# Kernel tuning notes

Measured on AMD Instinct MI355X. Metric: run time of the kernel, lower is better.

The kernel has to match this reference:

```python
import jax, jax.numpy as jnp
import numpy as np

B, S, D, H, F = 4, 1024, 512, 8, 2048
EPS = 1e-6


def _layernorm(x, g, b):
    m = jnp.mean(x, axis=-1, keepdims=True)
    v = jnp.mean(jnp.square(x - m), axis=-1, keepdims=True)
    return (x - m) * jax.lax.rsqrt(v + EPS) * g + b


def setup_inputs() -> dict:
    key = jax.random.key(0)
    ks = jax.random.split(key, 16)
    sd = 0.02
    return {
        "input_tensor": jax.random.normal(ks[0], (B, S, D), jnp.float32),
        # per-head QKV projections: each head maps D -> D (full depth, as in source)
        "Wq": jax.random.normal(ks[1], (H, D, D), jnp.float32) * sd,
        "bq": jnp.zeros((H, D), jnp.float32),
        "Wk": jax.random.normal(ks[2], (H, D, D), jnp.float32) * sd,
        "bk": jnp.zeros((H, D), jnp.float32),
        "Wv": jax.random.normal(ks[3], (H, D, D), jnp.float32) * sd,
        "bv": jnp.zeros((H, D), jnp.float32),
        # output projection after concat of H full-depth heads: (H*D) -> D
        "Wo": jax.random.normal(ks[4], (H * D, D), jnp.float32) * sd,
        "bo": jnp.zeros((D,), jnp.float32),
        "g1": jnp.ones((D,), jnp.float32),
        "beta1": jnp.zeros((D,), jnp.float32),
        "W1": jax.random.normal(ks[5], (D, F), jnp.float32) * sd,
        "b1": jnp.zeros((F,), jnp.float32),
        "W2": jax.random.normal(ks[6], (F, D), jnp.float32) * sd,
        "b2": jnp.zeros((D,), jnp.float32),
        "g2": jnp.ones((D,), jnp.float32),
        "beta2": jnp.zeros((D,), jnp.float32),
    }


def reference(input_tensor, Wq, bq, Wk, bk, Wv, bv, Wo, bo,
              g1, beta1, W1, b1, W2, b2, g2, beta2):
    x = input_tensor
    # batched per-head projections: [B,S,D] x [H,D,E] -> [B,H,S,E]
    q = jnp.einsum("bsd,hde->bhse", x, Wq) + bq[None, :, None, :]
    k = jnp.einsum("bsd,hde->bhse", x, Wk) + bk[None, :, None, :]
    v = jnp.einsum("bsd,hde->bhse", x, Wv) + bv[None, :, None, :]
    scale = 1.0 / jnp.sqrt(jnp.asarray(D, x.dtype))
    scores = jnp.einsum("bhse,bhte->bhst", q, k) * scale  # [B,H,S,S]
    attn = jax.nn.softmax(scores, axis=-1)
    heads = jnp.einsum("bhst,bhte->bhse", attn, v)  # [B,H,S,E]
    # concat heads on last axis: [B,S,H*D]
    concat = jnp.transpose(heads, (0, 2, 1, 3)).reshape(B, S, H * D)
    mha = concat @ Wo + bo  # [B,S,D]
    # dropout is identity at inference
    y = _layernorm(x + mha, g1, beta1)
    ff = jax.nn.relu(y @ W1 + b1) @ W2 + b2
    return _layernorm(y + ff, g2, beta2)
```

## Files before the change

kernel.cpp:

```cpp
#include <hip/hip_runtime.h>
#include <hip/hip_bf16.h>

typedef unsigned short u16;
typedef unsigned int u32;
typedef __attribute__((ext_vector_type(4))) float f32x4;
typedef __attribute__((ext_vector_type(8))) __bf16 bf16x8;

#define DEV __device__ __forceinline__

DEV u16 f2bf(float f) {
  union { float f; unsigned u; } c; c.f = f;
  unsigned r = (c.u + 0x7fffu + ((c.u >> 16) & 1u)) >> 16;
  return (u16)r;
}

DEV float bf2f(u16 u) {
  union { u32 u; float f; } c; c.u = (u32)u << 16;
  return c.f;
}

DEV void gld_lds16(const void* g, void* l) {
  __builtin_amdgcn_global_load_lds(
      (__attribute__((address_space(1))) void*)g,
      (__attribute__((address_space(3))) void*)l, 16, 0, 0);
}

DEV f32x4 mfma_bf16(bf16x8 a, bf16x8 b, f32x4 c) {
  return __builtin_amdgcn_mfma_f32_16x16x32_bf16(a, b, c, 0, 0, 0);
}

DEV void bar_vm0() { asm volatile("s_waitcnt vmcnt(0) lgkmcnt(0)\n\ts_barrier" ::: "memory"); }
DEV void wait_lg0() { asm volatile("s_waitcnt lgkmcnt(0)" ::: "memory"); }

DEV u32 cvt_pk_bf16(float lo, float hi) {
  u32 d;
  asm("v_cvt_pk_bf16_f32 %0, %1, %2" : "=v"(d) : "v"(lo), "v"(hi));
  return d;
}

__global__ __launch_bounds__(256) void prep_kernel(const float* __restrict__ x,
                                                   const float* __restrict__ Wq,
                                                   const float* __restrict__ Wk,
                                                   const float* __restrict__ Wv,
                                                   const float* __restrict__ Wo,
                                                   const float* __restrict__ W1,
                                                   const float* __restrict__ W2,
                                                   u16* __restrict__ xb, u16* __restrict__ wqC,
                                                   u16* __restrict__ wkC, u16* __restrict__ wvC,
                                                   u16* __restrict__ woT, u16* __restrict__ w1T,
                                                   u16* __restrict__ w2T) {
  int b = blockIdx.x;
  int tid = threadIdx.x;
  if (b < 8192) {
    const float* in;
    u16* out;
    int i;
    if (b < 2048) { in = x; out = xb; i = b * 256 + tid; }
    else {
      int idx = b - 2048;
      int job = idx >> 11;
      in = job == 0 ? Wq : (job == 1 ? Wk : Wv);
      out = job == 0 ? wqC : (job == 1 ? wkC : wvC);
      i = (idx & 2047) * 256 + tid;
    }
    float4 v = ((const float4*)in)[i];
    ushort4 o;
    o.x = f2bf(v.x); o.y = f2bf(v.y); o.z = f2bf(v.z); o.w = f2bf(v.w);
    ((ushort4*)out)[i] = o;
    return;
  }
  int idx = b - 8192;
  const float* in;
  u16* out;
  int R, C, bx, by;
  if (idx < 2048) { in = Wo; out = woT; R = 4096; C = 512; by = idx >> 4; bx = idx & 15; }
  else if (idx < 3072) { int rr = idx - 2048; in = W1; out = w1T; R = 512; C = 2048; by = rr >> 6; bx = rr & 63; }
  else { int rr = idx - 3072; in = W2; out = w2T; R = 2048; C = 512; by = rr >> 4; bx = rr & 15; }
  __shared__ float t[32][33];
  int c0 = bx * 32, r0 = by * 32;
  int tx = tid & 31, ty = tid >> 5;
#pragma unroll
  for (int i = 0; i < 4; ++i) {
    int rr2 = ty + i * 8;
    t[rr2][tx] = in[(size_t)(r0 + rr2) * C + c0 + tx];
  }
  __syncthreads();
#pragma unroll
  for (int i = 0; i < 4; ++i) {
    int cc = ty + i * 8;
    out[(size_t)(c0 + cc) * R + r0 + tx] = f2bf(t[tx][cc]);
  }
}

__global__ __launch_bounds__(256) void biasp_kernel(const float* __restrict__ Wo,
                                                    const float* __restrict__ bv,
                                                    float* __restrict__ biasP) {
  int b = blockIdx.x;
  int h = b >> 2, ec = b & 3;
  int t = threadIdx.x;
  int tl = t & 127, half = t >> 7;
  int e = ec * 128 + tl;
  float acc = 0.f;
  for (int i = 0; i < 256; ++i) {
    int e2 = half * 256 + i;
    acc += Wo[(size_t)(h * 512 + e2) * 512 + e] * bv[h * 512 + e2];
  }
  __shared__ float sh[2][128];
  sh[half][tl] = acc;
  __syncthreads();
  if (half == 0) biasP[h * 512 + e] = sh[0][tl] + sh[1][tl];
}

template <int AMODE>
__global__ __launch_bounds__(256) void gemm_bat(const u16* __restrict__ A,
                                                const u16* __restrict__ B,
                                                u16* __restrict__ out) {
  constexpr int BK = 64, BM = 128, BN = 128;
  __shared__ u16 As[2][BM * BK];
  __shared__ u16 Bs[2][BN * BK];
  const int tid = threadIdx.x;
  const int wave = tid >> 6, lane = tid & 63;
  const int r = lane & 15, g = lane >> 4;
  const int row0 = blockIdx.y * BM, col0 = blockIdx.x * BN;
  const int head = row0 >> 9;
  const int wr = (wave >> 1) * 64, wc = (wave & 1) * 64;

  auto stage = [&](int kt, int p) {
#pragma unroll
    for (int i = 0; i < 4; ++i) {
      int bi = i * 256 + wave * 64;
      int c = bi + lane;
      int row = c >> 3, ch = (c & 7) ^ (row & 7);
      size_t aoff;
      if constexpr (AMODE == 0)
        aoff = (size_t)(row0 + row) * 512 + kt + ch * 8;
      else
        aoff = (size_t)((row0 + row) & 511) * 4096 + head * 512 + kt + ch * 8;
      gld_lds16(A + aoff, &As[p][(size_t)bi * 8]);
    }
#pragma unroll
    for (int i = 0; i < 4; ++i) {
      int bi = i * 256 + wave * 64;
      int c = bi + lane;
      int row = c >> 3, ch = (c & 7) ^ (row & 7);
      gld_lds16(B + (size_t)(head * 512 + col0 + row) * 512 + kt + ch * 8,
                &Bs[p][(size_t)bi * 8]);
    }
  };

  f32x4 acc[4][4] = {};
  stage(0, 0);
  for (int t = 0; t < 8; ++t) {
    const int p = t & 1;
    bar_vm0();
    if (t < 7) stage((t + 1) * BK, p ^ 1);
    __builtin_amdgcn_s_setprio(1);
#pragma unroll
    for (int kk = 0; kk < 2; ++kk) {
      bf16x8 af[4], bfv[4];
#pragma unroll
      for (int m = 0; m < 4; ++m)
        af[m] = *(const bf16x8*)(&As[p][(wr + m * 16 + r) * BK + (((kk * 4 + g) ^ (r & 7))) * 8]);
#pragma unroll
      for (int n = 0; n < 4; ++n)
        bfv[n] = *(const bf16x8*)(&Bs[p][(wc + n * 16 + r) * BK + (((kk * 4 + g) ^ (r & 7))) * 8]);
#pragma unroll
      for (int m = 0; m < 4; ++m)
#pragma unroll
        for (int n = 0; n < 4; ++n)
          acc[m][n] = mfma_bf16(af[m], bfv[n], acc[m][n]);
    }
    __builtin_amdgcn_s_setprio(0);
  }
#pragma unroll
  for (int m = 0; m < 4; ++m)
#pragma unroll
    for (int n = 0; n < 4; ++n)
#pragma unroll
      for (int j = 0; j < 4; ++j)
        out[(size_t)(row0 + wr + m * 16 + g * 4 + j) * 512 + col0 + wc + n * 16 + r] =
            f2bf(acc[m][n][j]);
}

template <int NT, int BM, int BN, int WM, int WN, int MODE, int SPLITK>
__global__ __launch_bounds__(NT) void gemm_tn(const u16* __restrict__ A,
                                              const u16* __restrict__ B, int N, int K,
                                              void* __restrict__ out0, void* __restrict__ out1,
                                              const float* __restrict__ bias0,
                                              const float* __restrict__ bias1) {
  constexpr int BK = 64;
  constexpr int MF = WM / 16, NF = WN / 16;
  constexpr int WC = BN / WN;
  constexpr int AI = (BM * BK / 8) / NT;
  constexpr int BI = (BN * BK / 8) / NT;
  __shared__ u16 As[2][BM * BK];
  __shared__ u16 Bs[2][BN * BK];
  const int tid = threadIdx.x;
  const int wave = tid >> 6, lane = tid & 63;
  const int r = lane & 15, g = lane >> 4;
  const int row0 = blockIdx.y * BM, col0 = blockIdx.x * BN;
  const int wr = (wave / WC) * WM, wc = (wave % WC) * WN;
  const int KS = K * SPLITK;
  const int kb0 = blockIdx.z * K;

  auto stage = [&](int kt, int p) {
#pragma unroll
    for (int i = 0; i < AI; ++i) {
      int bi = i * NT + wave * 64;
      int c = bi + lane;
      int row = c >> 3, ch = (c & 7) ^ (row & 7);
      gld_lds16(A + (size_t)(row0 + row) * KS + kb0 + kt + ch * 8, &As[p][(size_t)bi * 8]);
    }
#pragma unroll
    for (int i = 0; i < BI; ++i) {
      int bi = i * NT + wave * 64;
      int c = bi + lane;
      int row = c >> 3, ch = (c & 7) ^ (row & 7);
      gld_lds16(B + (size_t)(col0 + row) * KS + kb0 + kt + ch * 8, &Bs[p][(size_t)bi * 8]);
    }
  };

  f32x4 acc[MF][NF] = {};
  const int nt = K / BK;

  stage(0, 0);
  for (int t = 0; t < nt; ++t) {
    const int p = t & 1;
    bar_vm0();
    if (t + 1 < nt) stage((t + 1) * BK, p ^ 1);
    __builtin_amdgcn_s_setprio(1);
#pragma unroll
    for (int kk = 0; kk < 2; ++kk) {
      bf16x8 af[MF], bfv[NF];
#pragma unroll
      for (int m = 0; m < MF; ++m)
        af[m] = *(const bf16x8*)(&As[p][(wr + m * 16 + r) * BK + (((kk * 4 + g) ^ (r & 7))) * 8]);
#pragma unroll
      for (int n = 0; n < NF; ++n)
        bfv[n] = *(const bf16x8*)(&Bs[p][(wc + n * 16 + r) * BK + (((kk * 4 + g) ^ (r & 7))) * 8]);
#pragma unroll
      for (int m = 0; m < MF; ++m)
#pragma unroll
        for (int n = 0; n < NF; ++n)
          acc[m][n] = mfma_bf16(af[m], bfv[n], acc[m][n]);
    }
    __builtin_amdgcn_s_setprio(0);
  }

  const size_t moff = (size_t)blockIdx.z * gridDim.y * BM * N;
#pragma unroll
  for (int m = 0; m < MF; ++m) {
#pragma unroll
    for (int n = 0; n < NF; ++n) {
      int gcol = col0 + wc + n * 16 + r;
#pragma unroll
      for (int j = 0; j < 4; ++j) {
        int grow = row0 + wr + m * 16 + g * 4 + j;
        float val = acc[m][n][j];
        if constexpr (MODE == 0) {
          int he = gcol;
          val += bias0[he];
          int bb = grow >> 10, s = grow & 1023;
          size_t off = (((size_t)(bb * 8 + (he >> 9)) * 1024 + s) * 512) + (he & 511);
          ((u16*)out0)[off] = f2bf(val);
        } else if constexpr (MODE == 1) {
          val += bias0[grow];
          int bb = gcol >> 10, s = gcol & 1023;
          size_t off = (((size_t)bb * 8 + (grow >> 9)) * 512 + (grow & 511)) * 1024 + s;
          ((u16*)out0)[off] = f2bf(val);
        } else if constexpr (MODE == 2) {
          if (SPLITK == 1 || blockIdx.z == 0) val += bias0[gcol];
          ((float*)out0)[moff + (size_t)grow * N + gcol] = val;
        } else {
          float v2 = fmaxf(val + bias0[gcol], 0.0f);
          ((u16*)out0)[(size_t)grow * N + gcol] = f2bf(v2);
        }
      }
    }
  }
  (void)out1; (void)bias1;
}

__global__ __launch_bounds__(512, 2) void flash_kernel(const u16* __restrict__ qg,
                                                       const u16* __restrict__ kg,
                                                       const u16* __restrict__ vtg,
                                                       u16* __restrict__ concat) {
  constexpr float SCALE = 0.04419417382415922f;
  __shared__ u16 Ks[2][32 * 512];
  __shared__ u16 Vs[2][32 * 512];
  __shared__ u32 PsU[8][256];

  const int tid = threadIdx.x;
  const int wave = tid >> 6, lane = tid & 63;
  const int r = lane & 15, g = lane >> 4;
  const int bx = blockIdx.x;
  const int xcd = bx & 7, slot = bx >> 3;
  const int bh = xcd * 4 + (slot >> 3);
  const int qt = slot & 7;
  const int bb = bh >> 3, hh = bh & 7;
  const size_t hbase = (size_t)bh * 1024 * 512;
  const u16* qp = qg + hbase;
  const u16* kp = kg + (size_t)bb * 1024 * 512;
  const u16* vp = vtg + hbase;
  const int q0 = qt * 128;

  bf16x8 q[16];
#pragma unroll
  for (int kk = 0; kk < 16; ++kk)
    q[kk] = *(const bf16x8*)(qp + (size_t)(q0 + wave * 16 + r) * 512 + kk * 32 + g * 8);

  const int krow8 = lane >> 3, kch = (lane & 7) ^ (lane >> 3);
  const int vrow4 = lane >> 2, vch = (lane & 3) ^ ((lane >> 3) & 3);
  auto stageKV = [&](int t, int p) {
    int kv = t * 32;
#pragma unroll
    for (int j = 0; j < 4; ++j) {
      int id = wave * 4 + j;
      gld_lds16(kp + (size_t)(kv + j * 8 + krow8) * 512 + wave * 64 + kch * 8,
                &Ks[p][id * 512]);
    }
#pragma unroll
    for (int j = 0; j < 4; ++j) {
      int n = wave * 4 + j;
      gld_lds16(vp + (size_t)(n * 16 + vrow4) * 1024 + kv + vch * 8, &Vs[p][n * 512]);
    }
  };

  f32x4 o[32] = {};
  float mrun = -1e30f, lrun = 0.f;

  stageKV(0, 0);

  const int krh = (r >> 3) * 512;
  const int ke0 = (r & 7) * 64 + ((g ^ (r & 7)) * 8);
  const int ke1 = (r & 7) * 64 + (((4 + g) ^ (r & 7)) * 8);
  const int voff = (r * 4 + (g ^ ((r >> 1) & 3))) * 8;

  for (int t = 0; t < 32; ++t) {
    const int p = t & 1;
    bar_vm0();
    if (t < 31) stageKV(t + 1, p ^ 1);

    __builtin_amdgcn_s_setprio(1);
    f32x4 a0 = {}, a1 = {}, b0 = {}, b1 = {};
#pragma unroll
    for (int kc = 0; kc < 8; ++kc) {
      const u16* kb = &Ks[p][kc * 2048 + krh];
      bf16x8 kf00 = *(const bf16x8*)(kb + ke0);
      bf16x8 kf01 = *(const bf16x8*)(kb + 1024 + ke0);
      bf16x8 kf10 = *(const bf16x8*)(kb + ke1);
      bf16x8 kf11 = *(const bf16x8*)(kb + 1024 + ke1);
      a0 = mfma_bf16(kf00, q[2 * kc], a0);
      b0 = mfma_bf16(kf01, q[2 * kc], b0);
      a1 = mfma_bf16(kf10, q[2 * kc + 1], a1);
      b1 = mfma_bf16(kf11, q[2 * kc + 1], b1);
    }
    __builtin_amdgcn_s_setprio(0);
    f32x4 s0 = a0 + a1;
    f32x4 s1 = b0 + b1;

    float m8 = -1e30f;
#pragma unroll
    for (int j = 0; j < 4; ++j) {
      s0[j] *= SCALE;
      s1[j] *= SCALE;
      m8 = fmaxf(m8, fmaxf(s0[j], s1[j]));
    }
    m8 = fmaxf(m8, __shfl_xor(m8, 16));
    m8 = fmaxf(m8, __shfl_xor(m8, 32));
    if (__any(m8 - mrun > 6.0f)) {
      float mn = fmaxf(mrun, m8);
      float rs = __expf(mrun - mn);
      mrun = mn;
      lrun *= rs;
#pragma unroll
      for (int j = 0; j < 4; ++j) {
        float rsj = __shfl(rs, (lane & 48) | (g * 4 + j));
#pragma unroll
        for (int n = 0; n < 32; ++n) o[n][j] *= rsj;
      }
    }
    f32x4 p0, p1;
    float ls = 0.f;
#pragma unroll
    for (int j = 0; j < 4; ++j) {
      p0[j] = __expf(s0[j] - mrun);
      p1[j] = __expf(s1[j] - mrun);
      ls += p0[j] + p1[j];
    }
    ls += __shfl_xor(ls, 16);
    ls += __shfl_xor(ls, 32);
    lrun += ls;

    {
      u32* pw = &PsU[wave][0];
      int base = r * 4 + (g & 1) * 2 + (g >> 1) * 64;
      pw[base + 0] = cvt_pk_bf16(p0[0], p0[1]);
      pw[base + 1] = cvt_pk_bf16(p0[2], p0[3]);
      pw[base + 128 + 0] = cvt_pk_bf16(p1[0], p1[1]);
      pw[base + 128 + 1] = cvt_pk_bf16(p1[2], p1[3]);
    }
    wait_lg0();

    bf16x8 pa = *(const bf16x8*)&PsU[wave][lane * 4];
    __builtin_amdgcn_s_setprio(1);
#pragma unroll
    for (int n = 0; n < 32; ++n) {
      bf16x8 bv = *(const bf16x8*)&Vs[p][n * 512 + voff];
      o[n] = mfma_bf16(pa, bv, o[n]);
    }
    __builtin_amdgcn_s_setprio(0);
  }

  float invl = 1.0f / lrun;
#pragma unroll
  for (int j = 0; j < 4; ++j) {
    float inv = __shfl(invl, (lane & 48) | (g * 4 + j));
    int srow = q0 + wave * 16 + g * 4 + j;
    size_t rowoff = ((size_t)bb * 1024 + srow) * 4096;
#pragma unroll
    for (int n = 0; n < 32; ++n) {
      int ocol = hh * 512 + n * 16 + r;
      concat[rowoff + ocol] = f2bf(o[n][j] * inv);
    }
  }
}

__global__ __launch_bounds__(128) void add_ln_kernel(const float* __restrict__ xin,
                                                     const u16* __restrict__ cc8,
                                                     const float* __restrict__ addin,
                                                     const float* __restrict__ addin2,
                                                     const float* __restrict__ bias,
                                                     const float* __restrict__ gamma,
                                                     const float* __restrict__ beta,
                                                     float* __restrict__ yout,
                                                     u16* __restrict__ ybout) {
  int row = blockIdx.x;
  int t = threadIdx.x;
  float4 xv = ((const float4*)(xin + (size_t)row * 512))[t];
  float v0 = xv.x, v1 = xv.y, v2 = xv.z, v3 = xv.w;
  if (cc8) {
    const u16* cr = cc8 + (size_t)row * 4096 + t * 4;
#pragma unroll
    for (int h = 0; h < 8; ++h) {
      ushort4 u = *(const ushort4*)(cr + h * 512);
      v0 += bf2f(u.x); v1 += bf2f(u.y); v2 += bf2f(u.z); v3 += bf2f(u.w);
    }
  }
  if (addin) {
    float4 av = ((const float4*)(addin + (size_t)row * 512))[t];
    v0 += av.x; v1 += av.y; v2 += av.z; v3 += av.w;
  }
  if (addin2) {
    float4 bv2 = ((const float4*)(addin2 + (size_t)row * 512))[t];
    v0 += bv2.x; v1 += bv2.y; v2 += bv2.z; v3 += bv2.w;
  }
  if (bias) {
    float4 b4 = ((const float4*)bias)[t];
    v0 += b4.x; v1 += b4.y; v2 += b4.z; v3 += b4.w;
  }
  float s1 = v0 + v1 + v2 + v3;
  float s2 = v0 * v0 + v1 * v1 + v2 * v2 + v3 * v3;
#pragma unroll
  for (int d = 1; d < 64; d <<= 1) {
    s1 += __shfl_xor(s1, d);
    s2 += __shfl_xor(s2, d);
  }
  __shared__ float sh[4];
  int wv = t >> 6;
  if ((t & 63) == 0) { sh[wv * 2] = s1; sh[wv * 2 + 1] = s2; }
  __syncthreads();
  s1 = sh[0] + sh[2];
  s2 = sh[1] + sh[3];
  float mean = s1 * (1.0f / 512.0f);
  float var = s2 * (1.0f / 512.0f) - mean * mean;
  float rstd = rsqrtf(var + 1e-6f);
  float4 gv = ((const float4*)gamma)[t];
  float4 bv = ((const float4*)beta)[t];
  float o0 = (v0 - mean) * rstd * gv.x + bv.x;
  float o1 = (v1 - mean) * rstd * gv.y + bv.y;
  float o2 = (v2 - mean) * rstd * gv.z + bv.z;
  float o3 = (v3 - mean) * rstd * gv.w + bv.w;
  float4 ov; ov.x = o0; ov.y = o1; ov.z = o2; ov.w = o3;
  ((float4*)(yout + (size_t)row * 512))[t] = ov;
  if (ybout) {
    ushort4 ub;
    ub.x = f2bf(o0); ub.y = f2bf(o1); ub.z = f2bf(o2); ub.w = f2bf(o3);
    ((ushort4*)(ybout + (size_t)row * 512))[t] = ub;
  }
}

extern "C" void kernel_launch(void* const* d_in, const int* in_sizes, int n_in, void* d_out,
                              int out_size, void* d_ws, size_t ws_size, hipStream_t stream) {
  (void)in_sizes; (void)n_in; (void)out_size; (void)ws_size;
  const float* x   = (const float*)d_in[0];
  const float* Wq  = (const float*)d_in[1];
  const float* bq  = (const float*)d_in[2];
  const float* Wk  = (const float*)d_in[3];
  const float* bk  = (const float*)d_in[4];
  const float* Wv  = (const float*)d_in[5];
  const float* bv  = (const float*)d_in[6];
  const float* Wo  = (const float*)d_in[7];
  const float* bo  = (const float*)d_in[8];
  const float* g1  = (const float*)d_in[9];
  const float* be1 = (const float*)d_in[10];
  const float* W1  = (const float*)d_in[11];
  const float* b1  = (const float*)d_in[12];
  const float* W2  = (const float*)d_in[13];
  const float* b2  = (const float*)d_in[14];
  const float* g2  = (const float*)d_in[15];
  const float* be2 = (const float*)d_in[16];
  (void)bk;

  char* ws = (char*)d_ws;
  const size_t MB = 1024 * 1024;
  u16*   xb    = (u16*)(ws + 0);
  u16*   wqC   = (u16*)(ws + 4 * MB);
  u16*   wkC   = (u16*)(ws + 8 * MB);
  u16*   wvC   = (u16*)(ws + 12 * MB);
  u16*   woT   = (u16*)(ws + 16 * MB);
  u16*   w1T   = (u16*)(ws + 20 * MB);
  u16*   w2T   = (u16*)(ws + 22 * MB);
  float* biasP = (float*)(ws + 24 * MB);
  u16*   mhT   = (u16*)(ws + 26 * MB);
  u16*   nhT   = (u16*)(ws + 30 * MB);
  u16*   qb    = (u16*)(ws + 34 * MB);
  u16*   vTb   = (u16*)(ws + 66 * MB);
  u16*   cc    = (u16*)(ws + 98 * MB);
  float* y     = (float*)(ws + 4 * MB);
  u16*   yb    = (u16*)(ws + 26 * MB);
  u16*   ff1   = (u16*)(ws + 34 * MB);
  float* ff2a  = (float*)(ws + 50 * MB);
  float* ff2b  = (float*)(ws + 58 * MB);

  prep_kernel<<<12288, 256, 0, stream>>>(x, Wq, Wk, Wv, Wo, W1, W2, xb, wqC, wkC, wvC,
                                         woT, w1T, w2T);
  biasp_kernel<<<32, 256, 0, stream>>>(Wo, bv, biasP);
  gemm_bat<0><<<dim3(4, 32), 256, 0, stream>>>(wkC, wqC, mhT);
  gemm_bat<1><<<dim3(4, 32), 256, 0, stream>>>(woT, wvC, nhT);
  gemm_tn<512, 256, 256, 128, 64, 0, 1><<<dim3(16, 16), 512, 0, stream>>>(xb, mhT, 4096, 512, qb, nullptr, bq, nullptr);
  gemm_tn<512, 256, 256, 128, 64, 1, 1><<<dim3(16, 16), 512, 0, stream>>>(nhT, xb, 4096, 512, vTb, nullptr, biasP, nullptr);
  flash_kernel<<<256, 512, 0, stream>>>(qb, xb, vTb, cc);
  add_ln_kernel<<<4096, 128, 0, stream>>>(x, cc, nullptr, nullptr, bo, g1, be1, y, yb);
  gemm_tn<256, 128, 128, 64, 64, 3, 1><<<dim3(16, 32), 256, 0, stream>>>(yb, w1T, 2048, 512, ff1, nullptr, b1, nullptr);
  gemm_tn<256, 64, 128, 32, 64, 2, 2><<<dim3(4, 64, 2), 256, 0, stream>>>(ff1, w2T, 512, 1024, ff2a, nullptr, b2, nullptr);
  add_ln_kernel<<<4096, 128, 0, stream>>>(y, nullptr, ff2a, ff2b, nullptr, g2, be2, (float*)d_out, nullptr);
}
```

Measured before the change: 247.1 us.

## Use FP8 for V and softmax probabilities in flash attention PV matmul

The V projection GEMM now writes its transposed output as FP8 bytes instead of bf16. The flash kernel stages V into a half-size LDS buffer with a new swizzle, packs the probabilities P to FP8, and uses the 16x16x32 fp8 MFMA for the P·V product. This halves V traffic and LDS footprint and uses the faster fp8 matrix path. The cost is precision: FP8 probabilities and V values may raise the error against the fp32 reference.

```diff
diff --git a/kernel.cpp b/kernel.cpp
--- a/kernel.cpp
+++ b/kernel.cpp
@@ -2,7 +2,9 @@
 #include <hip/hip_bf16.h>
 
 typedef unsigned short u16;
+typedef unsigned char u8;
 typedef unsigned int u32;
+typedef long long i64;
 typedef __attribute__((ext_vector_type(4))) float f32x4;
 typedef __attribute__((ext_vector_type(8))) __bf16 bf16x8;
 
@@ -32,10 +34,15 @@
 DEV void bar_vm0() { asm volatile("s_waitcnt vmcnt(0) lgkmcnt(0)\n\ts_barrier" ::: "memory"); }
 DEV void wait_lg0() { asm volatile("s_waitcnt lgkmcnt(0)" ::: "memory"); }
 
-DEV u32 cvt_pk_bf16(float lo, float hi) {
-  u32 d;
-  asm("v_cvt_pk_bf16_f32 %0, %1, %2" : "=v"(d) : "v"(lo), "v"(hi));
-  return d;
+DEV u32 pack_fp8x4(float a, float b, float c, float d) {
+  u32 t = __builtin_amdgcn_cvt_pk_fp8_f32(a, b, 0, false);
+  t = __builtin_amdgcn_cvt_pk_fp8_f32(c, d, t, true);
+  return t;
+}
+
+DEV u8 f2fp8(float v) {
+  u32 t = __builtin_amdgcn_cvt_pk_fp8_f32(v, v, 0, false);
+  return (u8)(t & 0xff);
 }
 
 __global__ __launch_bounds__(256) void prep_kernel(const float* __restrict__ x,
@@ -185,9 +192,8 @@
 template <int NT, int BM, int BN, int WM, int WN, int MODE, int SPLITK>
 __global__ __launch_bounds__(NT) void gemm_tn(const u16* __restrict__ A,
                                               const u16* __restrict__ B, int N, int K,
-                                              void* __restrict__ out0, void* __restrict__ out1,
-                                              const float* __restrict__ bias0,
-                                              const float* __restrict__ bias1) {
+                                              void* __restrict__ out0,
+                                              const float* __restrict__ bias0) {
   constexpr int BK = 64;
   constexpr int MF = WM / 16, NF = WN / 16;
   constexpr int WC = BN / WN;
@@ -267,7 +273,7 @@
           val += bias0[grow];
           int bb = gcol >> 10, s = gcol & 1023;
           size_t off = (((size_t)bb * 8 + (grow >> 9)) * 512 + (grow & 511)) * 1024 + s;
-          ((u16*)out0)[off] = f2bf(val);
+          ((u8*)out0)[off] = f2fp8(val);
         } else if constexpr (MODE == 2) {
           if (SPLITK == 1 || blockIdx.z == 0) val += bias0[gcol];
           ((float*)out0)[moff + (size_t)grow * N + gcol] = val;
@@ -278,17 +284,16 @@
       }
     }
   }
-  (void)out1; (void)bias1;
 }
 
 __global__ __launch_bounds__(512, 2) void flash_kernel(const u16* __restrict__ qg,
                                                        const u16* __restrict__ kg,
-                                                       const u16* __restrict__ vtg,
+                                                       const u8* __restrict__ vtg,
                                                        u16* __restrict__ concat) {
   constexpr float SCALE = 0.04419417382415922f;
   __shared__ u16 Ks[2][32 * 512];
-  __shared__ u16 Vs[2][32 * 512];
-  __shared__ u32 PsU[8][256];
+  __shared__ __align__(16) u8 VsB[2][16 * 1024];
+  __shared__ __align__(16) u32 PsP[8][128];
 
   const int tid = threadIdx.x;
   const int wave = tid >> 6, lane = tid & 63;
@@ -301,7 +306,7 @@
   const size_t hbase = (size_t)bh * 1024 * 512;
   const u16* qp = qg + hbase;
   const u16* kp = kg + (size_t)bb * 1024 * 512;
-  const u16* vp = vtg + hbase;
+  const u8* vp = vtg + (size_t)bh * 512 * 1024;
   const int q0 = qt * 128;
 
   bf16x8 q[16];
@@ -310,7 +315,9 @@
     q[kk] = *(const bf16x8*)(qp + (size_t)(q0 + wave * 16 + r) * 512 + kk * 32 + g * 8);
 
   const int krow8 = lane >> 3, kch = (lane & 7) ^ (lane >> 3);
-  const int vrow4 = lane >> 2, vch = (lane & 3) ^ ((lane >> 3) & 3);
+  const int vrow_s = lane >> 1;
+  const int vsw_s = (vrow_s & 2) ^ ((vrow_s >> 2) & 2);
+  const int vhalf = lane & 1;
   auto stageKV = [&](int t, int p) {
     int kv = t * 32;
 #pragma unroll
@@ -320,9 +327,10 @@
                 &Ks[p][id * 512]);
     }
 #pragma unroll
-    for (int j = 0; j < 4; ++j) {
-      int n = wave * 4 + j;
-      gld_lds16(vp + (size_t)(n * 16 + vrow4) * 1024 + kv + vch * 8, &Vs[p][n * 512]);
+    for (int jj = 0; jj < 2; ++jj) {
+      int nv = wave * 2 + jj;
+      gld_lds16(vp + (size_t)(nv * 32 + vrow_s) * 1024 + kv + (((vhalf * 2) ^ vsw_s) * 8),
+                &VsB[p][nv * 1024]);
     }
   };
 
@@ -334,7 +342,9 @@
   const int krh = (r >> 3) * 512;
   const int ke0 = (r & 7) * 64 + ((g ^ (r & 7)) * 8);
   const int ke1 = (r & 7) * 64 + (((4 + g) ^ (r & 7)) * 8);
-  const int voff = (r * 4 + (g ^ ((r >> 1) & 3))) * 8;
+  const int vsw = (r & 2) ^ ((r >> 2) & 2);
+  const int vo8 = ((g ^ vsw) << 3);
+  const int psw = r & 6;
 
   for (int t = 0; t < 32; ++t) {
     const int p = t & 1;
@@ -393,21 +403,21 @@
     lrun += ls;
 
     {
-      u32* pw = &PsU[wave][0];
-      int base = r * 4 + (g & 1) * 2 + (g >> 1) * 64;
-      pw[base + 0] = cvt_pk_bf16(p0[0], p0[1]);
-      pw[base + 1] = cvt_pk_bf16(p0[2], p0[3]);
-      pw[base + 128 + 0] = cvt_pk_bf16(p1[0], p1[1]);
-      pw[base + 128 + 1] = cvt_pk_bf16(p1[2], p1[3]);
+      u32* pw = PsP[wave];
+      u32 wA = pack_fp8x4(p0[0], p0[1], p0[2], p0[3]);
+      u32 wB = pack_fp8x4(p1[0], p1[1], p1[2], p1[3]);
+      pw[r * 8 + (g ^ psw)] = wA;
+      pw[r * 8 + ((4 + g) ^ psw)] = wB;
     }
     wait_lg0();
 
-    bf16x8 pa = *(const bf16x8*)&PsU[wave][lane * 4];
+    i64 pa = *(const i64*)&PsP[wave][r * 8 + ((2 * g) ^ psw)];
     __builtin_amdgcn_s_setprio(1);
 #pragma unroll
     for (int n = 0; n < 32; ++n) {
-      bf16x8 bv = *(const bf16x8*)&Vs[p][n * 512 + voff];
-      o[n] = mfma_bf16(pa, bv, o[n]);
+      int vrow = ((n & 1) << 4) + r;
+      i64 bv = *(const i64*)&VsB[p][((n >> 1) << 10) + vrow * 32 + vo8];
+      o[n] = __builtin_amdgcn_mfma_f32_16x16x32_fp8_fp8(pa, bv, o[n], 0, 0, 0);
     }
     __builtin_amdgcn_s_setprio(0);
   }
@@ -525,7 +535,7 @@
   u16*   mhT   = (u16*)(ws + 26 * MB);
   u16*   nhT   = (u16*)(ws + 30 * MB);
   u16*   qb    = (u16*)(ws + 34 * MB);
-  u16*   vTb   = (u16*)(ws + 66 * MB);
+  u8*    vTb   = (u8*)(ws + 66 * MB);
   u16*   cc    = (u16*)(ws + 98 * MB);
   float* y     = (float*)(ws + 4 * MB);
   u16*   yb    = (u16*)(ws + 26 * MB);
@@ -538,11 +548,11 @@
   biasp_kernel<<<32, 256, 0, stream>>>(Wo, bv, biasP);
   gemm_bat<0><<<dim3(4, 32), 256, 0, stream>>>(wkC, wqC, mhT);
   gemm_bat<1><<<dim3(4, 32), 256, 0, stream>>>(woT, wvC, nhT);
-  gemm_tn<512, 256, 256, 128, 64, 0, 1><<<dim3(16, 16), 512, 0, stream>>>(xb, mhT, 4096, 512, qb, nullptr, bq, nullptr);
-  gemm_tn<512, 256, 256, 128, 64, 1, 1><<<dim3(16, 16), 512, 0, stream>>>(nhT, xb, 4096, 512, vTb, nullptr, biasP, nullptr);
+  gemm_tn<512, 256, 256, 128, 64, 0, 1><<<dim3(16, 16), 512, 0, stream>>>(xb, mhT, 4096, 512, qb, bq);
+  gemm_tn<512, 256, 256, 128, 64, 1, 1><<<dim3(16, 16), 512, 0, stream>>>(nhT, xb, 4096, 512, vTb, biasP);
   flash_kernel<<<256, 512, 0, stream>>>(qb, xb, vTb, cc);
   add_ln_kernel<<<4096, 128, 0, stream>>>(x, cc, nullptr, nullptr, bo, g1, be1, y, yb);
-  gemm_tn<256, 128, 128, 64, 64, 3, 1><<<dim3(16, 32), 256, 0, stream>>>(yb, w1T, 2048, 512, ff1, nullptr, b1, nullptr);
-  gemm_tn<256, 64, 128, 32, 64, 2, 2><<<dim3(4, 64, 2), 256, 0, stream>>>(ff1, w2T, 512, 1024, ff2a, nullptr, b2, nullptr);
+  gemm_tn<256, 128, 128, 64, 64, 3, 1><<<dim3(16, 32), 256, 0, stream>>>(yb, w1T, 2048, 512, ff1, b1);
+  gemm_tn<256, 64, 128, 32, 64, 2, 2><<<dim3(4, 64, 2), 256, 0, stream>>>(ff1, w2T, 512, 1024, ff2a, b2);
   add_ln_kernel<<<4096, 128, 0, stream>>>(y, nullptr, ff2a, ff2b, nullptr, g2, be2, (float*)d_out, nullptr);
 }
```

Measured after the change: 250.0 us. About the same (+1.2%).
